# Kernel optimization log

Measured on AMD Instinct MI355X. Metric: run time of the kernel, lower is better.

The kernel has to match this reference:

```python
import jax, jax.numpy as jnp
import numpy as np

B, D, L, H = 2048, 64, 64, 512  # batch, in_dim, latent_space, hidden


def setup_inputs() -> dict:
    key = jax.random.key(0)
    ks = jax.random.split(key, 12)
    inp = {
        "x": jax.random.normal(ks[0], (B, D), jnp.float32),
        "koopman": jax.random.normal(ks[1], (B, L, D), jnp.float32),
    }
    dims = [(L, H), (H, H), (H, H), (H, D)]
    k = 2
    for pfx in ("s", "t"):
        for j, (fi, fo) in enumerate(dims):
            inp[f"{pfx}W{j+1}"] = jax.random.normal(ks[k], (fi, fo), jnp.float32) / np.sqrt(fi).astype(np.float32)
            inp[f"{pfx}b{j+1}"] = jnp.zeros((fo,), jnp.float32)
            k += 1
    return inp


def _mlp(z, W1, b1, W2, b2, W3, b3, W4, b4):
    h = jnp.tanh(z @ W1 + b1)
    h = jnp.tanh(h @ W2 + b2)
    h = jnp.tanh(h @ W3 + b3)
    return h @ W4 + b4


def reference(x, koopman,
              sW1, sb1, sW2, sb2, sW3, sb3, sW4, sb4,
              tW1, tb1, tW2, tb2, tW3, tb3, tW4, tb4):
    # koopman: (B, L, D) -> z: (B, D, L); column i of the torch loop is z[:, i, :]
    z = jnp.swapaxes(koopman, 1, 2)
    s = _mlp(z, sW1, sb1, sW2, sb2, sW3, sb3, sW4, sb4)  # (B, D, D)
    t = _mlp(z, tW1, tb1, tW2, tb2, tW3, tb3, tW4, tb4)  # (B, D, D)
    # loop kept only output column i for input column i -> diagonal over last two dims
    ds = jnp.diagonal(s, axis1=1, axis2=2)  # (B, D)
    dt = jnp.diagonal(t, axis1=1, axis2=2)  # (B, D)
    return (x - dt) * jnp.exp(-ds)
```

## Files before the change

kernel.cpp:

```cpp
#include <hip/hip_runtime.h>


typedef _Float16 f16;
typedef _Float16 f16x8 __attribute__((ext_vector_type(8)));
typedef float f32x4 __attribute__((ext_vector_type(4)));

#define WPACK_PER_NET 589824
#define OFF_W1 0
#define OFF_W2 32768
#define OFF_W3 294912
#define OFF_W4T 557056
#define WPACK_BYTES (2u * WPACK_PER_NET * sizeof(f16))

__global__ void pack_weights(const float* __restrict__ sW1, const float* __restrict__ sW2,
                             const float* __restrict__ sW3, const float* __restrict__ sW4,
                             const float* __restrict__ tW1, const float* __restrict__ tW2,
                             const float* __restrict__ tW3, const float* __restrict__ tW4,
                             f16* __restrict__ dst) {
  int idx = blockIdx.x * 256 + threadIdx.x;
  if (idx >= 2 * WPACK_PER_NET) return;
  int net = idx >= WPACK_PER_NET;
  int f = idx - net * WPACK_PER_NET;
  const float* W1 = net ? tW1 : sW1;
  const float* W2 = net ? tW2 : sW2;
  const float* W3 = net ? tW3 : sW3;
  const float* W4 = net ? tW4 : sW4;
  float v;
  if (f < OFF_W2) {
    int j = f & 7, lane = (f >> 3) & 63, nt = (f >> 9) & 31, kk = f >> 14;
    v = W1[(kk * 32 + (lane >> 4) * 8 + j) * 512 + nt * 16 + (lane & 15)];
  } else if (f < OFF_W3) {
    int f2 = f - OFF_W2;
    int j = f2 & 7, lane = (f2 >> 3) & 63, nt = (f2 >> 9) & 31, kk = f2 >> 14;
    v = W2[(kk * 32 + (lane >> 4) * 8 + j) * 512 + nt * 16 + (lane & 15)];
  } else if (f < OFF_W4T) {
    int f3 = f - OFF_W3;
    int j = f3 & 7, lane = (f3 >> 3) & 63, nt = (f3 >> 9) & 31, kk = f3 >> 14;
    v = W3[(kk * 32 + (lane >> 4) * 8 + j) * 512 + nt * 16 + (lane & 15)];
  } else {
    int f4 = f - OFF_W4T;
    v = W4[(f4 & 511) * 64 + (f4 >> 9)];
  }
  dst[net * WPACK_PER_NET + f] = (f16)v;
}

__device__ __forceinline__ int aidx(int m, int k) {
  return (((k >> 5) * 4 + (m >> 4)) * 64 + (m & 15) + ((k >> 3) & 3) * 16) * 8 + (k & 7);
}

__device__ __forceinline__ float fast_tanh(float x) {
  float e = __expf(x + x);
  return fmaf(-2.0f, __builtin_amdgcn_rcpf(e + 1.0f), 1.0f);
}

template <bool PACKED>
__device__ __forceinline__ void load_b(const f16* __restrict__ Wblk,
                                       const float* __restrict__ Wraw,
                                       int kk, int wave, int lane, f16x8* bdst) {
  if (PACKED) {
#pragma unroll
    for (int nt = 0; nt < 4; nt++)
      bdst[nt] = *(const f16x8*)(Wblk + kk * 16384 + ((wave * 4 + nt) * 64 + lane) * 8);
  } else {
    int n0 = wave * 64 + (lane & 15);
    int kb = kk * 32 + (lane >> 4) * 8;
#pragma unroll
    for (int nt = 0; nt < 4; nt++) {
      f16x8 v;
#pragma unroll
      for (int j = 0; j < 8; j++) v[j] = (f16)Wraw[(kb + j) * 512 + n0 + nt * 16];
      bdst[nt] = v;
    }
  }
}

template <int NS, bool PACKED>
__device__ __forceinline__ void mlp_layer(const f16* __restrict__ Wblk,
                                          const float* __restrict__ Wraw,
                                          const float* __restrict__ bias,
                                          const f16* Asrc, f16* Hout,
                                          int wave, int lane, int sbase) {
  f32x4 acc[4][4];
#pragma unroll
  for (int nt = 0; nt < 4; nt++) {
    float bv = bias[wave * 64 + nt * 16 + (lane & 15)];
#pragma unroll
    for (int mt = 0; mt < 4; mt++) acc[mt][nt] = f32x4{bv, bv, bv, bv};
  }

  f16x8 bb[2][4];
  load_b<PACKED>(Wblk, Wraw, 0, wave, lane, bb[0]);
#pragma unroll
  for (int kk = 0; kk < NS; kk++) {
    if (kk + 1 < NS) load_b<PACKED>(Wblk, Wraw, kk + 1, wave, lane, bb[(kk + 1) & 1]);
    const f16* ab = Asrc + kk * 2048 + lane * 8;
    f16x8 a[4];
#pragma unroll
    for (int mt = 0; mt < 4; mt++) a[mt] = *(const f16x8*)(ab + mt * 512);
#pragma unroll
    for (int mt = 0; mt < 4; mt++)
#pragma unroll
      for (int nt = 0; nt < 4; nt++)
        acc[mt][nt] = __builtin_amdgcn_mfma_f32_16x16x32_f16(a[mt], bb[kk & 1][nt],
                                                             acc[mt][nt], 0, 0, 0);
  }
  __syncthreads();

  f16* hb = Hout + sbase;
#pragma unroll
  for (int mt = 0; mt < 4; mt++)
#pragma unroll
    for (int nt = 0; nt < 4; nt++)
#pragma unroll
      for (int r = 0; r < 4; r++)
        hb[(nt >> 1) * 2048 + mt * 512 + (nt & 1) * 256 + r * 8] =
            (f16)fast_tanh(acc[mt][nt][r]);
  __syncthreads();
}

template <bool PACKED>
__global__ __launch_bounds__(512, 4) void decoder_main(
    const float* __restrict__ x, const float* __restrict__ koop,
    const f16* __restrict__ wpack,
    const float* __restrict__ sW1, const float* __restrict__ sW2,
    const float* __restrict__ sW3, const float* __restrict__ sW4,
    const float* __restrict__ tW1, const float* __restrict__ tW2,
    const float* __restrict__ tW3, const float* __restrict__ tW4,
    const float* __restrict__ sb1, const float* __restrict__ sb2,
    const float* __restrict__ sb3, const float* __restrict__ sb4,
    const float* __restrict__ tb1, const float* __restrict__ tb2,
    const float* __restrict__ tb3, const float* __restrict__ tb4,
    float* __restrict__ out) {
  __shared__ __align__(16) f16 ZA[4096];
  __shared__ __align__(16) f16 HA[32768];
  __shared__ float redBuf[2][64];

  const int b = blockIdx.x;
  const int t = threadIdx.x;
  const int wave = t >> 6, lane = t & 63;
  const int sbase =
      wave * 4096 + (lane >> 4) * 32 + ((lane & 15) >> 3) * 128 + (lane & 7);

  const float* kb = koop + b * 4096;
#pragma unroll
  for (int i = 0; i < 8; i++) {
    int flat = t + 512 * i;
    ZA[aidx(flat & 63, flat >> 6)] = (f16)kb[flat];
  }
  __syncthreads();

  for (int net = 0; net < 2; net++) {
    const f16* wb = PACKED ? (wpack + net * WPACK_PER_NET) : (const f16*)0;
    const float* W1 = net ? tW1 : sW1;
    const float* W2 = net ? tW2 : sW2;
    const float* W3 = net ? tW3 : sW3;
    const float* W4 = net ? tW4 : sW4;
    const float* b1 = net ? tb1 : sb1;
    const float* b2 = net ? tb2 : sb2;
    const float* b3 = net ? tb3 : sb3;
    const float* b4 = net ? tb4 : sb4;
    mlp_layer<2, PACKED>(PACKED ? wb + OFF_W1 : 0, W1, b1, ZA, HA, wave, lane, sbase);
    mlp_layer<16, PACKED>(PACKED ? wb + OFF_W2 : 0, W2, b2, HA, HA, wave, lane, sbase);
    mlp_layer<16, PACKED>(PACKED ? wb + OFF_W3 : 0, W3, b3, HA, HA, wave, lane, sbase);

    int i = t >> 3, sub = t & 7;
    float p = 0.f;
#pragma unroll
    for (int q = 0; q < 8; q++) {
      int k0 = sub * 64 + q * 8;
      f16x8 hv = *(const f16x8*)&HA[aidx(i, k0)];
      if (PACKED) {
        f16x8 wv = *(const f16x8*)&wb[OFF_W4T + i * 512 + k0];
#pragma unroll
        for (int j = 0; j < 8; j++) p += (float)hv[j] * (float)wv[j];
      } else {
#pragma unroll
        for (int j = 0; j < 8; j++) p += (float)hv[j] * W4[(k0 + j) * 64 + i];
      }
    }
    p += __shfl_down(p, 4, 8);
    p += __shfl_down(p, 2, 8);
    p += __shfl_down(p, 1, 8);
    if (sub == 0) redBuf[net][i] = p + b4[i];
    __syncthreads();
  }

  if (t < 64) {
    out[b * 64 + t] = (x[b * 64 + t] - redBuf[1][t]) * __expf(-redBuf[0][t]);
  }
}

extern "C" void kernel_launch(void* const* d_in, const int* in_sizes, int n_in,
                              void* d_out, int out_size, void* d_ws, size_t ws_size,
                              hipStream_t stream) {
  const float* x    = (const float*)d_in[0];
  const float* koop = (const float*)d_in[1];
  const float* sW1 = (const float*)d_in[2];  const float* sb1 = (const float*)d_in[3];
  const float* sW2 = (const float*)d_in[4];  const float* sb2 = (const float*)d_in[5];
  const float* sW3 = (const float*)d_in[6];  const float* sb3 = (const float*)d_in[7];
  const float* sW4 = (const float*)d_in[8];  const float* sb4 = (const float*)d_in[9];
  const float* tW1 = (const float*)d_in[10]; const float* tb1 = (const float*)d_in[11];
  const float* tW2 = (const float*)d_in[12]; const float* tb2 = (const float*)d_in[13];
  const float* tW3 = (const float*)d_in[14]; const float* tb3 = (const float*)d_in[15];
  const float* tW4 = (const float*)d_in[16]; const float* tb4 = (const float*)d_in[17];
  float* out = (float*)d_out;

  if (ws_size >= (size_t)WPACK_BYTES) {
    f16* wpack = (f16*)d_ws;
    pack_weights<<<4608, 256, 0, stream>>>(sW1, sW2, sW3, sW4, tW1, tW2, tW3, tW4, wpack);
    decoder_main<true><<<2048, 512, 0, stream>>>(
        x, koop, wpack, sW1, sW2, sW3, sW4, tW1, tW2, tW3, tW4,
        sb1, sb2, sb3, sb4, tb1, tb2, tb3, tb4, out);
  } else {
    decoder_main<false><<<2048, 512, 0, stream>>>(
        x, koop, (const f16*)0, sW1, sW2, sW3, sW4, tW1, tW2, tW3, tW4,
        sb1, sb2, sb3, sb4, tb1, tb2, tb3, tb4, out);
  }
}
```

Measured before the change: 431.8 us.

## Prefetch weights through a cross-layer register ring and coalesce weight packing

Replaces the per-layer double-buffered weight loads with a 4-slot register ring that prefetches weight half-tiles four steps ahead, continuing across layer and network boundaries via a shared-memory offset table. The aim is to hide global-memory latency at layer starts instead of stalling after each barrier. The packing kernel is rewritten to stage each weight slab through shared memory so global reads and writes are coalesced. Barriers become a custom waitcnt plus s_barrier; this adds register pressure and relies on the inline-asm barrier being sufficient for ordering.

```diff
diff --git a/kernel.cpp b/kernel.cpp
--- a/kernel.cpp
+++ b/kernel.cpp
@@ -12,36 +12,55 @@
 #define OFF_W4T 557056
 #define WPACK_BYTES (2u * WPACK_PER_NET * sizeof(f16))
 
-__global__ void pack_weights(const float* __restrict__ sW1, const float* __restrict__ sW2,
-                             const float* __restrict__ sW3, const float* __restrict__ sW4,
-                             const float* __restrict__ tW1, const float* __restrict__ tW2,
-                             const float* __restrict__ tW3, const float* __restrict__ tW4,
-                             f16* __restrict__ dst) {
-  int idx = blockIdx.x * 256 + threadIdx.x;
-  if (idx >= 2 * WPACK_PER_NET) return;
-  int net = idx >= WPACK_PER_NET;
-  int f = idx - net * WPACK_PER_NET;
-  const float* W1 = net ? tW1 : sW1;
-  const float* W2 = net ? tW2 : sW2;
-  const float* W3 = net ? tW3 : sW3;
-  const float* W4 = net ? tW4 : sW4;
-  float v;
-  if (f < OFF_W2) {
-    int j = f & 7, lane = (f >> 3) & 63, nt = (f >> 9) & 31, kk = f >> 14;
-    v = W1[(kk * 32 + (lane >> 4) * 8 + j) * 512 + nt * 16 + (lane & 15)];
-  } else if (f < OFF_W3) {
-    int f2 = f - OFF_W2;
-    int j = f2 & 7, lane = (f2 >> 3) & 63, nt = (f2 >> 9) & 31, kk = f2 >> 14;
-    v = W2[(kk * 32 + (lane >> 4) * 8 + j) * 512 + nt * 16 + (lane & 15)];
-  } else if (f < OFF_W4T) {
-    int f3 = f - OFF_W3;
-    int j = f3 & 7, lane = (f3 >> 3) & 63, nt = (f3 >> 9) & 31, kk = f3 >> 14;
-    v = W3[(kk * 32 + (lane >> 4) * 8 + j) * 512 + nt * 16 + (lane & 15)];
+__device__ __forceinline__ void lds_barrier() {
+  asm volatile("s_waitcnt lgkmcnt(0)\n\ts_barrier" ::: "memory");
+}
+
+__global__ __launch_bounds__(512) void pack_weights2(
+    const float* __restrict__ sW1, const float* __restrict__ sW2,
+    const float* __restrict__ sW3, const float* __restrict__ sW4,
+    const float* __restrict__ tW1, const float* __restrict__ tW2,
+    const float* __restrict__ tW3, const float* __restrict__ tW4,
+    f16* __restrict__ dst) {
+  __shared__ f16 sb[32768];
+  const int w = blockIdx.x, t = threadIdx.x;
+  if (w < 68) {
+    int net = w >= 34;
+    int s = w - net * 34;
+    int l = (s < 2) ? 0 : (s < 18 ? 1 : 2);
+    int kk = s - (l == 0 ? 0 : (l == 1 ? 2 : 18));
+    const float* W = l == 0 ? (net ? tW1 : sW1)
+                            : (l == 1 ? (net ? tW2 : sW2) : (net ? tW3 : sW3));
+    int lb = l == 0 ? OFF_W1 : (l == 1 ? OFF_W2 : OFF_W3);
+#pragma unroll
+    for (int i = 0; i < 32; i++) sb[i * 512 + t] = (f16)W[(kk * 32 + i) * 512 + t];
+    __syncthreads();
+    f16* db = dst + net * WPACK_PER_NET + lb + kk * 16384;
+#pragma unroll
+    for (int q = 0; q < 32; q++) {
+      int flat = q * 512 + t;
+      int w_ = flat >> 11, r2 = flat & 2047;
+      int p = r2 >> 10, nt2 = (r2 >> 9) & 1, ln = (r2 >> 3) & 63, j = r2 & 7;
+      int n = w_ * 64 + (p * 2 + nt2) * 16 + (ln & 15);
+      int kloc = (ln >> 4) * 8 + j;
+      db[flat] = sb[kloc * 512 + n];
+    }
   } else {
-    int f4 = f - OFF_W4T;
-    v = W4[(f4 & 511) * 64 + (f4 >> 9)];
-  }
-  dst[net * WPACK_PER_NET + f] = (f16)v;
+    int net = w - 68;
+    const float* W4 = net ? tW4 : sW4;
+#pragma unroll
+    for (int q = 0; q < 64; q++) {
+      int u = q * 512 + t;
+      sb[u] = (f16)W4[u];
+    }
+    __syncthreads();
+    f16* db = dst + net * WPACK_PER_NET + OFF_W4T;
+#pragma unroll
+    for (int q = 0; q < 64; q++) {
+      int d = q * 512 + t;
+      db[d] = sb[(d & 511) * 64 + (d >> 9)];
+    }
+  }
 }
 
 __device__ __forceinline__ int aidx(int m, int k) {
@@ -53,33 +72,11 @@
   return fmaf(-2.0f, __builtin_amdgcn_rcpf(e + 1.0f), 1.0f);
 }
 
-template <bool PACKED>
-__device__ __forceinline__ void load_b(const f16* __restrict__ Wblk,
-                                       const float* __restrict__ Wraw,
-                                       int kk, int wave, int lane, f16x8* bdst) {
-  if (PACKED) {
-#pragma unroll
-    for (int nt = 0; nt < 4; nt++)
-      bdst[nt] = *(const f16x8*)(Wblk + kk * 16384 + ((wave * 4 + nt) * 64 + lane) * 8);
-  } else {
-    int n0 = wave * 64 + (lane & 15);
-    int kb = kk * 32 + (lane >> 4) * 8;
-#pragma unroll
-    for (int nt = 0; nt < 4; nt++) {
-      f16x8 v;
-#pragma unroll
-      for (int j = 0; j < 8; j++) v[j] = (f16)Wraw[(kb + j) * 512 + n0 + nt * 16];
-      bdst[nt] = v;
-    }
-  }
-}
-
-template <int NS, bool PACKED>
-__device__ __forceinline__ void mlp_layer(const f16* __restrict__ Wblk,
-                                          const float* __restrict__ Wraw,
-                                          const float* __restrict__ bias,
-                                          const f16* Asrc, f16* Hout,
-                                          int wave, int lane, int sbase) {
+template <int NS>
+__device__ __forceinline__ void layer_ring(
+    const char* __restrict__ wb, const unsigned int* eoff, int estart,
+    f16x8 (&ring)[4][2], const float* __restrict__ bias,
+    const f16* Asrc, f16* Hout, int wave, int lane, int sbase, int laneoff) {
   f32x4 acc[4][4];
 #pragma unroll
   for (int nt = 0; nt < 4; nt++) {
@@ -87,12 +84,158 @@
 #pragma unroll
     for (int mt = 0; mt < 4; mt++) acc[mt][nt] = f32x4{bv, bv, bv, bv};
   }
-
+#pragma unroll
+  for (int kk = 0; kk < NS; kk++) {
+    const f16* ab = Asrc + kk * 2048 + lane * 8;
+    f16x8 a[4];
+#pragma unroll
+    for (int mt = 0; mt < 4; mt++) a[mt] = *(const f16x8*)(ab + mt * 512);
+#pragma unroll
+    for (int p = 0; p < 2; p++) {
+      const int slot = (2 * kk + p) & 3;
+      f16x8 b0 = ring[slot][0], b1 = ring[slot][1];
+      {
+        const char* gp = wb + eoff[estart + 2 * kk + p + 4] + laneoff;
+        ring[slot][0] = *(const f16x8*)gp;
+        ring[slot][1] = *(const f16x8*)(gp + 1024);
+      }
+#pragma unroll
+      for (int mt = 0; mt < 4; mt++) {
+        acc[mt][2 * p] = __builtin_amdgcn_mfma_f32_16x16x32_f16(
+            a[mt], b0, acc[mt][2 * p], 0, 0, 0);
+        acc[mt][2 * p + 1] = __builtin_amdgcn_mfma_f32_16x16x32_f16(
+            a[mt], b1, acc[mt][2 * p + 1], 0, 0, 0);
+      }
+    }
+  }
+  lds_barrier();
+  f16* hb = Hout + sbase;
+#pragma unroll
+  for (int mt = 0; mt < 4; mt++)
+#pragma unroll
+    for (int nt = 0; nt < 4; nt++)
+#pragma unroll
+      for (int r = 0; r < 4; r++)
+        hb[(nt >> 1) * 2048 + mt * 512 + (nt & 1) * 256 + r * 8] =
+            (f16)fast_tanh(acc[mt][nt][r]);
+  lds_barrier();
+}
+
+__global__ __launch_bounds__(512, 4) void decoder_ring(
+    const float* __restrict__ x, const float* __restrict__ koop,
+    const f16* __restrict__ wpack,
+    const float* __restrict__ sb1, const float* __restrict__ sb2,
+    const float* __restrict__ sb3, const float* __restrict__ sb4,
+    const float* __restrict__ tb1, const float* __restrict__ tb2,
+    const float* __restrict__ tb3, const float* __restrict__ tb4,
+    float* __restrict__ out) {
+  __shared__ __align__(16) f16 ZA[4096];
+  __shared__ __align__(16) f16 HA[32768];
+  __shared__ unsigned int eoff[144];
+  __shared__ float redBuf[2][64];
+
+  const int b = blockIdx.x;
+  const int t = threadIdx.x;
+  const int wave = t >> 6, lane = t & 63;
+  const int sbase =
+      wave * 4096 + (lane >> 4) * 32 + ((lane & 15) >> 3) * 128 + (lane & 7);
+  const int laneoff = wave * 4096 + lane * 16;
+
+  if (t < 144) {
+    unsigned int off = 0;
+    if (t < 136) {
+      int net = t >= 68;
+      int r = t - net * 68;
+      int l = (r < 4) ? 0 : (r < 36 ? 1 : 2);
+      int rr = r - (l == 0 ? 0 : (l == 1 ? 4 : 36));
+      int lb = (l == 0) ? OFF_W1 : (l == 1 ? OFF_W2 : OFF_W3);
+      off = (unsigned int)(net * WPACK_PER_NET + lb + (rr >> 1) * 16384 +
+                           (rr & 1) * 1024) * 2u;
+    }
+    eoff[t] = off;
+  }
+
+  const float* kb = koop + b * 4096;
+#pragma unroll
+  for (int i = 0; i < 8; i++) {
+    int flat = t + 512 * i;
+    ZA[aidx(flat & 63, flat >> 6)] = (f16)kb[flat];
+  }
+  __syncthreads();
+
+  const char* wb = (const char*)wpack;
+  f16x8 ring[4][2];
+#pragma unroll
+  for (int s = 0; s < 4; s++) {
+    const char* gp = wb + eoff[s] + laneoff;
+    ring[s][0] = *(const f16x8*)gp;
+    ring[s][1] = *(const f16x8*)(gp + 1024);
+  }
+
+#pragma unroll 1
+  for (int net = 0; net < 2; net++) {
+    const float* b1 = net ? tb1 : sb1;
+    const float* b2 = net ? tb2 : sb2;
+    const float* b3 = net ? tb3 : sb3;
+    const float* b4 = net ? tb4 : sb4;
+    const int e0 = net * 68;
+    layer_ring<2>(wb, eoff, e0, ring, b1, ZA, HA, wave, lane, sbase, laneoff);
+    layer_ring<16>(wb, eoff, e0 + 4, ring, b2, HA, HA, wave, lane, sbase, laneoff);
+    layer_ring<16>(wb, eoff, e0 + 36, ring, b3, HA, HA, wave, lane, sbase, laneoff);
+
+    const f16* w4t = wpack + net * WPACK_PER_NET + OFF_W4T;
+    int i = t >> 3, sub = t & 7;
+    float p = 0.f;
+#pragma unroll
+    for (int q = 0; q < 8; q++) {
+      int k0 = sub * 64 + q * 8;
+      f16x8 hv = *(const f16x8*)&HA[aidx(i, k0)];
+      f16x8 wv = *(const f16x8*)&w4t[i * 512 + k0];
+#pragma unroll
+      for (int j = 0; j < 8; j++) p += (float)hv[j] * (float)wv[j];
+    }
+    p += __shfl_down(p, 4, 8);
+    p += __shfl_down(p, 2, 8);
+    p += __shfl_down(p, 1, 8);
+    if (sub == 0) redBuf[net][i] = p + b4[i];
+    lds_barrier();
+  }
+
+  if (t < 64) {
+    out[b * 64 + t] = (x[b * 64 + t] - redBuf[1][t]) * __expf(-redBuf[0][t]);
+  }
+}
+
+__device__ __forceinline__ void load_b_direct(const float* __restrict__ Wraw,
+                                              int kk, int wave, int lane,
+                                              f16x8* bdst) {
+  int n0 = wave * 64 + (lane & 15);
+  int kb = kk * 32 + (lane >> 4) * 8;
+#pragma unroll
+  for (int nt = 0; nt < 4; nt++) {
+    f16x8 v;
+#pragma unroll
+    for (int j = 0; j < 8; j++) v[j] = (f16)Wraw[(kb + j) * 512 + n0 + nt * 16];
+    bdst[nt] = v;
+  }
+}
+
+template <int NS>
+__device__ __forceinline__ void mlp_layer_direct(
+    const float* __restrict__ Wraw, const float* __restrict__ bias,
+    const f16* Asrc, f16* Hout, int wave, int lane, int sbase) {
+  f32x4 acc[4][4];
+#pragma unroll
+  for (int nt = 0; nt < 4; nt++) {
+    float bv = bias[wave * 64 + nt * 16 + (lane & 15)];
+#pragma unroll
+    for (int mt = 0; mt < 4; mt++) acc[mt][nt] = f32x4{bv, bv, bv, bv};
+  }
   f16x8 bb[2][4];
-  load_b<PACKED>(Wblk, Wraw, 0, wave, lane, bb[0]);
+  load_b_direct(Wraw, 0, wave, lane, bb[0]);
 #pragma unroll
   for (int kk = 0; kk < NS; kk++) {
-    if (kk + 1 < NS) load_b<PACKED>(Wblk, Wraw, kk + 1, wave, lane, bb[(kk + 1) & 1]);
+    if (kk + 1 < NS) load_b_direct(Wraw, kk + 1, wave, lane, bb[(kk + 1) & 1]);
     const f16* ab = Asrc + kk * 2048 + lane * 8;
     f16x8 a[4];
 #pragma unroll
@@ -105,7 +248,6 @@
                                                              acc[mt][nt], 0, 0, 0);
   }
   __syncthreads();
-
   f16* hb = Hout + sbase;
 #pragma unroll
   for (int mt = 0; mt < 4; mt++)
@@ -118,10 +260,8 @@
   __syncthreads();
 }
 
-template <bool PACKED>
-__global__ __launch_bounds__(512, 4) void decoder_main(
+__global__ __launch_bounds__(512, 4) void decoder_direct(
     const float* __restrict__ x, const float* __restrict__ koop,
-    const f16* __restrict__ wpack,
     const float* __restrict__ sW1, const float* __restrict__ sW2,
     const float* __restrict__ sW3, const float* __restrict__ sW4,
     const float* __restrict__ tW1, const float* __restrict__ tW2,
@@ -134,13 +274,11 @@
   __shared__ __align__(16) f16 ZA[4096];
   __shared__ __align__(16) f16 HA[32768];
   __shared__ float redBuf[2][64];
-
   const int b = blockIdx.x;
   const int t = threadIdx.x;
   const int wave = t >> 6, lane = t & 63;
   const int sbase =
       wave * 4096 + (lane >> 4) * 32 + ((lane & 15) >> 3) * 128 + (lane & 7);
-
   const float* kb = koop + b * 4096;
 #pragma unroll
   for (int i = 0; i < 8; i++) {
@@ -148,9 +286,7 @@
     ZA[aidx(flat & 63, flat >> 6)] = (f16)kb[flat];
   }
   __syncthreads();
-
   for (int net = 0; net < 2; net++) {
-    const f16* wb = PACKED ? (wpack + net * WPACK_PER_NET) : (const f16*)0;
     const float* W1 = net ? tW1 : sW1;
     const float* W2 = net ? tW2 : sW2;
     const float* W3 = net ? tW3 : sW3;
@@ -159,24 +295,17 @@
     const float* b2 = net ? tb2 : sb2;
     const float* b3 = net ? tb3 : sb3;
     const float* b4 = net ? tb4 : sb4;
-    mlp_layer<2, PACKED>(PACKED ? wb + OFF_W1 : 0, W1, b1, ZA, HA, wave, lane, sbase);
-    mlp_layer<16, PACKED>(PACKED ? wb + OFF_W2 : 0, W2, b2, HA, HA, wave, lane, sbase);
-    mlp_layer<16, PACKED>(PACKED ? wb + OFF_W3 : 0, W3, b3, HA, HA, wave, lane, sbase);
-
+    mlp_layer_direct<2>(W1, b1, ZA, HA, wave, lane, sbase);
+    mlp_layer_direct<16>(W2, b2, HA, HA, wave, lane, sbase);
+    mlp_layer_direct<16>(W3, b3, HA, HA, wave, lane, sbase);
     int i = t >> 3, sub = t & 7;
     float p = 0.f;
 #pragma unroll
     for (int q = 0; q < 8; q++) {
       int k0 = sub * 64 + q * 8;
       f16x8 hv = *(const f16x8*)&HA[aidx(i, k0)];
-      if (PACKED) {
-        f16x8 wv = *(const f16x8*)&wb[OFF_W4T + i * 512 + k0];
-#pragma unroll
-        for (int j = 0; j < 8; j++) p += (float)hv[j] * (float)wv[j];
-      } else {
-#pragma unroll
-        for (int j = 0; j < 8; j++) p += (float)hv[j] * W4[(k0 + j) * 64 + i];
-      }
+#pragma unroll
+      for (int j = 0; j < 8; j++) p += (float)hv[j] * W4[(k0 + j) * 64 + i];
     }
     p += __shfl_down(p, 4, 8);
     p += __shfl_down(p, 2, 8);
@@ -184,7 +313,6 @@
     if (sub == 0) redBuf[net][i] = p + b4[i];
     __syncthreads();
   }
-
   if (t < 64) {
     out[b * 64 + t] = (x[b * 64 + t] - redBuf[1][t]) * __expf(-redBuf[0][t]);
   }
@@ -207,13 +335,14 @@
 
   if (ws_size >= (size_t)WPACK_BYTES) {
     f16* wpack = (f16*)d_ws;
-    pack_weights<<<4608, 256, 0, stream>>>(sW1, sW2, sW3, sW4, tW1, tW2, tW3, tW4, wpack);
-    decoder_main<true><<<2048, 512, 0, stream>>>(
-        x, koop, wpack, sW1, sW2, sW3, sW4, tW1, tW2, tW3, tW4,
+    pack_weights2<<<70, 512, 0, stream>>>(sW1, sW2, sW3, sW4, tW1, tW2, tW3, tW4,
+                                          wpack);
+    decoder_ring<<<2048, 512, 0, stream>>>(x, koop, wpack,
+                                           sb1, sb2, sb3, sb4,
+                                           tb1, tb2, tb3, tb4, out);
+  } else {
+    decoder_direct<<<2048, 512, 0, stream>>>(
+        x, koop, sW1, sW2, sW3, sW4, tW1, tW2, tW3, tW4,
         sb1, sb2, sb3, sb4, tb1, tb2, tb3, tb4, out);
-  } else {
-    decoder_main<false><<<2048, 512, 0, stream>>>(
-        x, koop, (const f16*)0, sW1, sW2, sW3, sW4, tW1, tW2, tW3, tW4,
-        sb1, sb2, sb3, sb4, tb1, tb2, tb3, tb4, out);
-  }
-}
+  }
+}
```

After: 487.6 us. +12.9%, slower.
